# Optimization experiments

Measured on AMD Instinct MI355X. Metric: run time of the kernel, lower is better.

The kernel has to match this reference:

```python
import jax, jax.numpy as jnp
import numpy as np

N = 2_000_000
CLAMP_THR = 0.9999999


def quat_to_rot(q):
    # q: [N,4] (unnormalized) -> [N,3,3] rotation matrices
    q = q / jnp.linalg.norm(q, axis=-1, keepdims=True)
    w, x, y, z = q[:, 0], q[:, 1], q[:, 2], q[:, 3]
    R = jnp.stack([
        jnp.stack([1 - 2 * (y * y + z * z), 2 * (x * y - w * z), 2 * (x * z + w * y)], axis=-1),
        jnp.stack([2 * (x * y + w * z), 1 - 2 * (x * x + z * z), 2 * (y * z - w * x)], axis=-1),
        jnp.stack([2 * (x * z - w * y), 2 * (y * z + w * x), 1 - 2 * (x * x + y * y)], axis=-1),
    ], axis=-2)
    return R


def setup_inputs() -> dict:
    key = jax.random.key(0)
    k1, k2, k3 = jax.random.split(key, 3)
    R_w2c1 = quat_to_rot(jax.random.normal(k1, (N, 4), dtype=jnp.float32))
    R_w2c2 = quat_to_rot(jax.random.normal(k2, (N, 4), dtype=jnp.float32))
    # small-angle noise rotation so residuals are realistic (cos inside clamp)
    q_noise = jnp.concatenate(
        [jnp.ones((N, 1), dtype=jnp.float32), 0.05 * jax.random.normal(k3, (N, 3), dtype=jnp.float32)],
        axis=-1)
    Rn = quat_to_rot(q_noise)
    # R_rel ~= R_w2c2 @ R_w2c1^T composed with noise
    R_rel = jnp.einsum('nij,njk->nik', jnp.einsum('nij,nkj->nik', R_w2c2, R_w2c1), Rn)
    return {"R_rel": R_rel, "R_w2c1": R_w2c1, "R_w2c2": R_w2c2}


def reference(R_rel, R_w2c1, R_w2c2):
    # residual M = R_rel^T @ R_w2c2 @ R_w2c1^T should be identity;
    # cos(theta) = (tr(M) - 1) / 2
    tr = jnp.einsum('nji,njk,nik->n', R_rel, R_w2c2, R_w2c1)
    cos = 0.5 * (tr - 1.0)
    cos_c = jnp.clip(cos, -CLAMP_THR, CLAMP_THR)
    loss = jnp.sum(jnp.arccos(cos_c))[None]  # shape (1,), matching the CUDA buffer
    # analytic gradient of sum arccos(cos) wrt R_w2c1, R_w2c2;
    # zero where the clamp is active (derivative of clip is 0 there)
    g = jnp.where(jnp.abs(cos) < CLAMP_THR,
                  -0.5 / jnp.sqrt(1.0 - cos_c * cos_c),
                  jnp.zeros_like(cos))  # includes d cos / d tr = 0.5
    # d tr / d R_w2c1 = R_rel^T @ R_w2c2 ; d tr / d R_w2c2 = R_rel @ R_w2c1
    d_R_w2c1 = g[:, None, None] * jnp.einsum('nji,njk->nik', R_rel, R_w2c2)
    d_R_w2c2 = g[:, None, None] * jnp.einsum('nij,njk->nik', R_rel, R_w2c1)
    return loss, d_R_w2c1, d_R_w2c2
```

## Files before the change

kernel.cpp:

```cpp
#include <hip/hip_runtime.h>

#define CLAMP_THR 0.9999999f

typedef float f4a __attribute__((ext_vector_type(4), aligned(4)));

__global__ void zero_loss_kernel(float* out) {
    if (threadIdx.x == 0) out[0] = 0.0f;
}

__device__ __forceinline__ float compute_store(
    const float R[9], const float A[9], const float B[9],
    float* __restrict__ o1, float* __restrict__ o2)
{
    float M[9];
    #pragma unroll
    for (int i = 0; i < 3; ++i)
        #pragma unroll
        for (int k = 0; k < 3; ++k)
            M[3 * i + k] = R[i]     * A[k]
                         + R[3 + i] * A[3 + k]
                         + R[6 + i] * A[6 + k];
    float tr = 0.0f;
    #pragma unroll
    for (int j = 0; j < 9; ++j) tr += M[j] * B[j];

    const float cosv = 0.5f * (tr - 1.0f);
    const float cosc = fminf(fmaxf(cosv, -CLAMP_THR), CLAMP_THR);
    const float g = (fabsf(cosv) < CLAMP_THR)
                      ? (-0.5f / sqrtf(1.0f - cosc * cosc))
                      : 0.0f;

    f4a s;
    s.x = g*M[0]; s.y = g*M[1]; s.z = g*M[2]; s.w = g*M[3];
    *(f4a*)(o1) = s;
    s.x = g*M[4]; s.y = g*M[5]; s.z = g*M[6]; s.w = g*M[7];
    *(f4a*)(o1 + 4) = s;
    o1[8] = g*M[8];

    float D[9];
    #pragma unroll
    for (int i = 0; i < 3; ++i)
        #pragma unroll
        for (int k = 0; k < 3; ++k)
            D[3 * i + k] = g * (R[3 * i]     * B[k]
                              + R[3 * i + 1] * B[3 + k]
                              + R[3 * i + 2] * B[6 + k]);
    s.x = D[0]; s.y = D[1]; s.z = D[2]; s.w = D[3];
    *(f4a*)(o2) = s;
    s.x = D[4]; s.y = D[5]; s.z = D[6]; s.w = D[7];
    *(f4a*)(o2 + 4) = s;
    o2[8] = D[8];

    return acosf(cosc);
}

template<bool USE_WS>
__global__ __launch_bounds__(256) void geodesic_ilp2_kernel(
    const float* __restrict__ Rrel,
    const float* __restrict__ Rw1,
    const float* __restrict__ Rw2,
    float* __restrict__ out,
    float* __restrict__ ws,
    int n)
{
    const int t    = threadIdx.x;
    const int lane = t & 63;
    const int w    = t >> 6;
    const int e0   = blockIdx.x * 512 + t;
    const int e1   = e0 + 256;

    float local_loss = 0.0f;
    float* __restrict__ out1 = out + 1;
    float* __restrict__ out2 = out + 1 + (size_t)n * 9;

    f4a r0a, r1a, a0a, a1a, b0a, b1a;  float r2a, a2a, b2a;
    f4a r0b, r1b, a0b, a1b, b0b, b1b;  float r2b, a2b, b2b;
    const bool va = (e0 < n), vb = (e1 < n);

    if (va) {
        const size_t b = (size_t)e0 * 9;
        r0a = *(const f4a*)(Rrel + b); r1a = *(const f4a*)(Rrel + b + 4); r2a = Rrel[b + 8];
        a0a = *(const f4a*)(Rw2  + b); a1a = *(const f4a*)(Rw2  + b + 4); a2a = Rw2[b + 8];
        b0a = *(const f4a*)(Rw1  + b); b1a = *(const f4a*)(Rw1  + b + 4); b2a = Rw1[b + 8];
    }
    if (vb) {
        const size_t b = (size_t)e1 * 9;
        r0b = *(const f4a*)(Rrel + b); r1b = *(const f4a*)(Rrel + b + 4); r2b = Rrel[b + 8];
        a0b = *(const f4a*)(Rw2  + b); a1b = *(const f4a*)(Rw2  + b + 4); a2b = Rw2[b + 8];
        b0b = *(const f4a*)(Rw1  + b); b1b = *(const f4a*)(Rw1  + b + 4); b2b = Rw1[b + 8];
    }

    if (va) {
        const size_t b = (size_t)e0 * 9;
        float R[9] = {r0a.x,r0a.y,r0a.z,r0a.w, r1a.x,r1a.y,r1a.z,r1a.w, r2a};
        float A[9] = {a0a.x,a0a.y,a0a.z,a0a.w, a1a.x,a1a.y,a1a.z,a1a.w, a2a};
        float B[9] = {b0a.x,b0a.y,b0a.z,b0a.w, b1a.x,b1a.y,b1a.z,b1a.w, b2a};
        local_loss += compute_store(R, A, B, out1 + b, out2 + b);
    }
    if (vb) {
        const size_t b = (size_t)e1 * 9;
        float R[9] = {r0b.x,r0b.y,r0b.z,r0b.w, r1b.x,r1b.y,r1b.z,r1b.w, r2b};
        float A[9] = {a0b.x,a0b.y,a0b.z,a0b.w, a1b.x,a1b.y,a1b.z,a1b.w, a2b};
        float B[9] = {b0b.x,b0b.y,b0b.z,b0b.w, b1b.x,b1b.y,b1b.z,b1b.w, b2b};
        local_loss += compute_store(R, A, B, out1 + b, out2 + b);
    }

    #pragma unroll
    for (int off = 32; off > 0; off >>= 1)
        local_loss += __shfl_down(local_loss, off, 64);
    if (lane == 0) {
        const int gw = blockIdx.x * 4 + w;
        if (USE_WS) ws[gw] = local_loss;
        else if (local_loss != 0.0f) atomicAdd(out, local_loss);
    }
}

__global__ __launch_bounds__(1024) void reduce_loss_kernel(
    const float* __restrict__ ws, int nw, float* __restrict__ out)
{
    __shared__ float wsum[16];
    const int t = threadIdx.x;
    float s = 0.0f;
    for (int i = t; i < nw; i += 1024) s += ws[i];
    #pragma unroll
    for (int off = 32; off > 0; off >>= 1)
        s += __shfl_down(s, off, 64);
    if ((t & 63) == 0) wsum[t >> 6] = s;
    __syncthreads();
    if (t == 0) {
        float tot = 0.0f;
        #pragma unroll
        for (int i = 0; i < 16; ++i) tot += wsum[i];
        out[0] = tot;
    }
}

extern "C" void kernel_launch(void* const* d_in, const int* in_sizes, int n_in,
                              void* d_out, int out_size, void* d_ws, size_t ws_size,
                              hipStream_t stream) {
    const float* Rrel = (const float*)d_in[0];
    const float* Rw1  = (const float*)d_in[1];
    const float* Rw2  = (const float*)d_in[2];
    float* out = (float*)d_out;
    const int n  = in_sizes[0] / 9;
    const int nb = (n + 511) / 512;
    const int nw = nb * 4;

    if (ws_size >= (size_t)nw * sizeof(float)) {
        geodesic_ilp2_kernel<true><<<nb, 256, 0, stream>>>(
            Rrel, Rw1, Rw2, out, (float*)d_ws, n);
        reduce_loss_kernel<<<1, 1024, 0, stream>>>((const float*)d_ws, nw, out);
    } else {
        zero_loss_kernel<<<1, 64, 0, stream>>>(out);
        geodesic_ilp2_kernel<false><<<nb, 256, 0, stream>>>(
            Rrel, Rw1, Rw2, out, nullptr, n);
    }
}
```

Baseline: 304.9 us.

## Stage input matrices through per-wave LDS for coalesced 16-byte loads

Each wave now loads its 64 matrices from each of the three inputs as fully coalesced contiguous float4 reads into a per-wave LDS buffer. After a wave-local fence, each lane reads back its own 9 floats. This replaces the strided per-thread 9-float loads, which used unaligned 16-byte accesses. The block now covers 256 elements, down from 512, which removes the two-element ILP per thread and doubles the grid. The change costs LDS traffic and capacity, and the output stores are still strided per thread.

```diff
diff --git a/kernel.cpp b/kernel.cpp
--- a/kernel.cpp
+++ b/kernel.cpp
@@ -2,10 +2,17 @@
 
 #define CLAMP_THR 0.9999999f
 
+typedef float f4  __attribute__((ext_vector_type(4)));
 typedef float f4a __attribute__((ext_vector_type(4), aligned(4)));
 
 __global__ void zero_loss_kernel(float* out) {
     if (threadIdx.x == 0) out[0] = 0.0f;
+}
+
+__device__ __forceinline__ void lds_fence() {
+    __builtin_amdgcn_wave_barrier();
+    asm volatile("s_waitcnt lgkmcnt(0)" ::: "memory");
+    __builtin_amdgcn_wave_barrier();
 }
 
 __device__ __forceinline__ float compute_store(
@@ -55,7 +62,7 @@
 }
 
 template<bool USE_WS>
-__global__ __launch_bounds__(256) void geodesic_ilp2_kernel(
+__global__ __launch_bounds__(256) void geodesic_wls_kernel(
     const float* __restrict__ Rrel,
     const float* __restrict__ Rw1,
     const float* __restrict__ Rw2,
@@ -63,46 +70,60 @@
     float* __restrict__ ws,
     int n)
 {
+    __shared__ float lds[4][3][576];
+
     const int t    = threadIdx.x;
     const int lane = t & 63;
     const int w    = t >> 6;
-    const int e0   = blockIdx.x * 512 + t;
-    const int e1   = e0 + 256;
+    const int E0   = (blockIdx.x * 4 + w) * 64;
 
     float local_loss = 0.0f;
     float* __restrict__ out1 = out + 1;
     float* __restrict__ out2 = out + 1 + (size_t)n * 9;
 
-    f4a r0a, r1a, a0a, a1a, b0a, b1a;  float r2a, a2a, b2a;
-    f4a r0b, r1b, a0b, a1b, b0b, b1b;  float r2b, a2b, b2b;
-    const bool va = (e0 < n), vb = (e1 < n);
+    if (E0 + 64 <= n) {
+        const size_t gbase = (size_t)E0 * 9;
+        const f4* __restrict__ gA = (const f4*)(Rrel + gbase);
+        const f4* __restrict__ gB = (const f4*)(Rw2  + gbase);
+        const f4* __restrict__ gC = (const f4*)(Rw1  + gbase);
+        const bool third = (lane < 16);
 
-    if (va) {
-        const size_t b = (size_t)e0 * 9;
-        r0a = *(const f4a*)(Rrel + b); r1a = *(const f4a*)(Rrel + b + 4); r2a = Rrel[b + 8];
-        a0a = *(const f4a*)(Rw2  + b); a1a = *(const f4a*)(Rw2  + b + 4); a2a = Rw2[b + 8];
-        b0a = *(const f4a*)(Rw1  + b); b1a = *(const f4a*)(Rw1  + b + 4); b2a = Rw1[b + 8];
-    }
-    if (vb) {
-        const size_t b = (size_t)e1 * 9;
-        r0b = *(const f4a*)(Rrel + b); r1b = *(const f4a*)(Rrel + b + 4); r2b = Rrel[b + 8];
-        a0b = *(const f4a*)(Rw2  + b); a1b = *(const f4a*)(Rw2  + b + 4); a2b = Rw2[b + 8];
-        b0b = *(const f4a*)(Rw1  + b); b1b = *(const f4a*)(Rw1  + b + 4); b2b = Rw1[b + 8];
-    }
+        f4 ra0 = gA[lane], rb0 = gB[lane], rc0 = gC[lane];
+        f4 ra1 = gA[64 + lane], rb1 = gB[64 + lane], rc1 = gC[64 + lane];
+        f4 ra2, rb2, rc2;
+        if (third) { ra2 = gA[128 + lane]; rb2 = gB[128 + lane]; rc2 = gC[128 + lane]; }
 
-    if (va) {
-        const size_t b = (size_t)e0 * 9;
-        float R[9] = {r0a.x,r0a.y,r0a.z,r0a.w, r1a.x,r1a.y,r1a.z,r1a.w, r2a};
-        float A[9] = {a0a.x,a0a.y,a0a.z,a0a.w, a1a.x,a1a.y,a1a.z,a1a.w, a2a};
-        float B[9] = {b0a.x,b0a.y,b0a.z,b0a.w, b1a.x,b1a.y,b1a.z,b1a.w, b2a};
-        local_loss += compute_store(R, A, B, out1 + b, out2 + b);
-    }
-    if (vb) {
-        const size_t b = (size_t)e1 * 9;
-        float R[9] = {r0b.x,r0b.y,r0b.z,r0b.w, r1b.x,r1b.y,r1b.z,r1b.w, r2b};
-        float A[9] = {a0b.x,a0b.y,a0b.z,a0b.w, a1b.x,a1b.y,a1b.z,a1b.w, a2b};
-        float B[9] = {b0b.x,b0b.y,b0b.z,b0b.w, b1b.x,b1b.y,b1b.z,b1b.w, b2b};
-        local_loss += compute_store(R, A, B, out1 + b, out2 + b);
+        f4* __restrict__ sA = (f4*)lds[w][0];
+        f4* __restrict__ sB = (f4*)lds[w][1];
+        f4* __restrict__ sC = (f4*)lds[w][2];
+        sA[lane] = ra0;       sB[lane] = rb0;       sC[lane] = rc0;
+        sA[64 + lane] = ra1;  sB[64 + lane] = rb1;  sC[64 + lane] = rc1;
+        if (third) { sA[128 + lane] = ra2; sB[128 + lane] = rb2; sC[128 + lane] = rc2; }
+        lds_fence();
+
+        const float* __restrict__ fA = lds[w][0] + 9 * lane;
+        const float* __restrict__ fB = lds[w][1] + 9 * lane;
+        const float* __restrict__ fC = lds[w][2] + 9 * lane;
+        float R[9], A[9], B[9];
+        #pragma unroll
+        for (int j = 0; j < 9; ++j) { R[j] = fA[j]; A[j] = fB[j]; B[j] = fC[j]; }
+
+        const size_t b = (size_t)(E0 + lane) * 9;
+        local_loss = compute_store(R, A, B, out1 + b, out2 + b);
+    } else if (E0 + lane < n) {
+        const size_t b = (size_t)(E0 + lane) * 9;
+        float R[9], A[9], B[9];
+        f4a v;
+        v = *(const f4a*)(Rrel + b);     R[0]=v.x; R[1]=v.y; R[2]=v.z; R[3]=v.w;
+        v = *(const f4a*)(Rrel + b + 4); R[4]=v.x; R[5]=v.y; R[6]=v.z; R[7]=v.w;
+        R[8] = Rrel[b + 8];
+        v = *(const f4a*)(Rw2 + b);      A[0]=v.x; A[1]=v.y; A[2]=v.z; A[3]=v.w;
+        v = *(const f4a*)(Rw2 + b + 4);  A[4]=v.x; A[5]=v.y; A[6]=v.z; A[7]=v.w;
+        A[8] = Rw2[b + 8];
+        v = *(const f4a*)(Rw1 + b);      B[0]=v.x; B[1]=v.y; B[2]=v.z; B[3]=v.w;
+        v = *(const f4a*)(Rw1 + b + 4);  B[4]=v.x; B[5]=v.y; B[6]=v.z; B[7]=v.w;
+        B[8] = Rw1[b + 8];
+        local_loss = compute_store(R, A, B, out1 + b, out2 + b);
     }
 
     #pragma unroll
@@ -143,16 +164,16 @@
     const float* Rw2  = (const float*)d_in[2];
     float* out = (float*)d_out;
     const int n  = in_sizes[0] / 9;
-    const int nb = (n + 511) / 512;
+    const int nb = (n + 255) / 256;
     const int nw = nb * 4;
 
     if (ws_size >= (size_t)nw * sizeof(float)) {
-        geodesic_ilp2_kernel<true><<<nb, 256, 0, stream>>>(
+        geodesic_wls_kernel<true><<<nb, 256, 0, stream>>>(
             Rrel, Rw1, Rw2, out, (float*)d_ws, n);
         reduce_loss_kernel<<<1, 1024, 0, stream>>>((const float*)d_ws, nw, out);
     } else {
         zero_loss_kernel<<<1, 64, 0, stream>>>(out);
-        geodesic_ilp2_kernel<false><<<nb, 256, 0, stream>>>(
+        geodesic_wls_kernel<false><<<nb, 256, 0, stream>>>(
             Rrel, Rw1, Rw2, out, nullptr, n);
     }
 }
```

Result: no change. 305.3 us (+0.1%).
